# Kernel optimization log

Measured on AMD Instinct MI355X. Metric: run time of the kernel, lower is better.

Reference implementation:

```python
import jax, jax.numpy as jnp
jax.config.update('jax_enable_x64', True)
import numpy as np

B = 16          # samples per batch
PTS = 50000     # points per sample
PP = 2048       # pairs per sample
C = 64          # backbone_out_channels
HID = 1024      # mlp_hidden
MASK = 65535
RANK_MSE_WEIGHT = 0.1


def _hash4(idx):
    # pack (b, x, y, z) into one int64 key, 16 bits per field
    idx = idx.astype(jnp.int64)
    return ((idx[:, 0] & MASK) << 48) | ((idx[:, 1] & MASK) << 32) | ((idx[:, 2] & MASK) << 16) | (idx[:, 3] & MASK)


def setup_inputs() -> dict:
    key = jax.random.key(0)
    ks = jax.random.split(key, 8)
    N = B * PTS
    P = B * PP
    grid_coord = jax.random.randint(ks[0], (N, 3), 0, 1024, dtype=jnp.int32)
    offset = (jnp.arange(1, B + 1) * PTS).astype(jnp.int64)          # cumulative point ends
    batch = jnp.searchsorted(offset, jnp.arange(N), side='right')
    point_indices = jnp.concatenate([batch[:, None].astype(jnp.int32), grid_coord], axis=1)
    perm = jax.random.permutation(ks[1], N)
    voxel_indices = point_indices[perm].astype(jnp.int64)            # backbone._last_indices
    voxel_features = jax.random.normal(ks[2], (N, C), dtype=jnp.float32)
    pairs = jax.random.randint(ks[3], (P, 2), 0, PTS, dtype=jnp.int64)   # sample-local indices
    pair_reward = jax.random.uniform(ks[4], (P,), dtype=jnp.float32)
    pair_offset = (jnp.arange(1, B + 1) * PP).astype(jnp.int64)      # cumulative pair ends
    din = 3 * C
    def lin(k, fi, fo):
        return jax.random.normal(k, (fi, fo), dtype=jnp.float32) / np.float32(np.sqrt(fi))
    W1 = lin(ks[5], din, HID); b1 = jnp.zeros((HID,), jnp.float32)
    W2 = lin(ks[6], HID, HID); b2 = jnp.zeros((HID,), jnp.float32)
    W3 = lin(ks[7], HID, 1);   b3 = jnp.zeros((1,), jnp.float32)
    return dict(voxel_features=voxel_features, pair_reward=pair_reward,
                W1=W1, b1=b1, W2=W2, b2=b2, W3=W3, b3=b3,
                grid_coord=grid_coord, offset=offset, voxel_indices=voxel_indices,
                pairs=pairs, pair_offset=pair_offset)


def reference(voxel_features, pair_reward, W1, b1, W2, b2, W3, b3,
              grid_coord, offset, voxel_indices, pairs, pair_offset):
    N = grid_coord.shape[0]
    # --- match sparse voxel features back to point order (sort + searchsorted + gather) ---
    batch = jnp.searchsorted(offset, jnp.arange(N), side='right')
    point_keys = _hash4(jnp.concatenate([batch[:, None].astype(jnp.int32), grid_coord], axis=1))
    voxel_keys = _hash4(voxel_indices)
    order = jnp.argsort(voxel_keys)
    vk_sorted = voxel_keys[order]
    loc = jnp.clip(jnp.searchsorted(vk_sorted, point_keys), 0, N - 1)
    point_feat = voxel_features[order[loc]]                          # [N, C]
    # --- shift sample-local pair indices by per-sample point start (vectorized offsets) ---
    P = pairs.shape[0]
    seg = jnp.searchsorted(pair_offset, jnp.arange(P), side='right') # segment id per pair
    point_starts = jnp.concatenate([jnp.zeros((1,), offset.dtype), offset[:-1]])
    shifted = pairs + point_starts[seg][:, None]
    f0 = point_feat[shifted[:, 0]]
    f1 = point_feat[shifted[:, 1]]
    pair_feat = jnp.concatenate([f0, f1, f0 - f1], axis=1)           # [P, 3C]
    # --- MLP head ---
    h = jax.nn.relu(pair_feat @ W1 + b1)
    h = jax.nn.relu(h @ W2 + b2)
    pred = (h @ W3 + b3)[:, 0]                                       # [P]
    # --- pair_rank loss, batched over equal-sized segments ---
    Bn = pair_offset.shape[0]
    Pp = P // Bn
    pb = pred.reshape(Bn, Pp)
    tb = pair_reward.reshape(Bn, Pp)
    dp = pb[:, :, None] - pb[:, None, :]                             # [B, Pp, Pp]
    dt = tb[:, :, None] - tb[:, None, :]
    sgn = jnp.sign(dt)
    triu = jnp.triu(jnp.ones((Pp, Pp), bool), 1)
    valid = triu[None, :, :] & (sgn != 0)
    sp = jax.nn.softplus(-sgn * dp)
    cnt = valid.sum(axis=(1, 2))
    rank_per = jnp.where(valid, sp, 0.0).sum(axis=(1, 2)) / jnp.maximum(cnt, 1)
    has = cnt > 0
    rank_loss = jnp.where(has, rank_per, 0.0).sum() / jnp.maximum(has.sum(), 1)
    mse_loss = jnp.mean((pb - tb) ** 2, axis=1).mean()
    loss = rank_loss + RANK_MSE_WEIGHT * mse_loss
    return loss
```

## Files before the change

### kernel.cpp

```cpp
#include <hip/hip_runtime.h>
#include <stdint.h>

#define BATCH   16
#define PTS     50000
#define PP      2048
#define NPTS    (BATCH*PTS)
#define NPAIR   (BATCH*PP)
#define NEND    (2*NPAIR)
#define CFEAT   64
#define KIN     128
#define HID     1024
#define QTS_LOG2 17
#define QTS     (1u<<QTS_LOG2)
#define QTS_MASK (QTS-1)
#define EMPTY_KEY 0xFFFFFFFFFFFFFFFFULL
#define NJB     64
#define RJ      (PP/NJB)

typedef unsigned long long ull;
typedef __attribute__((ext_vector_type(4))) float f32x4;
typedef __attribute__((ext_vector_type(8))) short bf16x8;

__device__ __forceinline__ ull mix64(ull h) {
  h ^= h >> 33; h *= 0xff51afd7ed558ccdULL;
  h ^= h >> 33; h *= 0xc4ceb9fe1a85ec53ULL;
  h ^= h >> 33; return h;
}

__device__ __forceinline__ unsigned short f2b(float x) {
  unsigned u = __float_as_uint(x);
  unsigned r = (u + 0x7FFFu + ((u >> 16) & 1u)) >> 16;
  return (unsigned short)r;
}

__global__ __launch_bounds__(256) void setup_kernel(
    ull* __restrict__ qtable, unsigned int* __restrict__ ans,
    const float* __restrict__ W1, unsigned short* __restrict__ Wt1,
    const float* __restrict__ W2, unsigned short* __restrict__ Wt2) {
  __shared__ unsigned short tile[32][33];
  int bid = blockIdx.x;
  int t = threadIdx.x;
  if (bid < 512) {
    int i = bid * 256 + t;
    qtable[i] = EMPTY_KEY;
    ans[i] = 0xFFFFFFFFu;
  } else if (bid < 1024) {
    int idx = (bid - 512) * 256 + t;
    int n = idx >> 7, k = idx & 127;
    float v;
    if (k < 64)
      v = W1[(size_t)k * HID + n] + W1[(size_t)(128 + k) * HID + n];
    else
      v = W1[(size_t)k * HID + n] - W1[(size_t)(64 + k) * HID + n];
    Wt1[(size_t)n * KIN + k] = f2b(v);
  } else {
    int b = bid - 1024;
    int nb = (b & 31) * 32, kb = (b >> 5) * 32;
    int tx = t & 31, ty = t >> 5;
#pragma unroll
    for (int r = 0; r < 32; r += 8)
      tile[ty + r][tx] = f2b(W2[(size_t)(kb + ty + r) * HID + nb + tx]);
    __syncthreads();
#pragma unroll
    for (int r = 0; r < 32; r += 8)
      Wt2[(size_t)(nb + ty + r) * HID + kb + tx] = tile[tx][ty + r];
  }
}

__global__ void qinsert(const int* __restrict__ pairs, const int* __restrict__ gc,
                        ull* __restrict__ qtable, unsigned int* __restrict__ eslot) {
  int e = blockIdx.x * blockDim.x + threadIdx.x;
  if (e >= NEND) return;
  int j = e >> 1, side = e & 1;
  int seg = j / PP;
  int pi = pairs[2*j + side] + seg * PTS;
  pi = pi < 0 ? 0 : (pi >= NPTS ? NPTS - 1 : pi);
  ull key = ((ull)seg << 30) | ((ull)(gc[3*pi] & 1023) << 20)
          | ((ull)(gc[3*pi+1] & 1023) << 10) | (ull)(gc[3*pi+2] & 1023);
  unsigned int h = (unsigned int)mix64(key) & QTS_MASK;
  for (int p = 0; p < (int)QTS; ++p) {
    ull prev = atomicCAS(&qtable[h], EMPTY_KEY, key);
    if (prev == EMPTY_KEY || prev == key) { eslot[e] = h; return; }
    h = (h + 1) & QTS_MASK;
  }
  eslot[e] = 0;
}

__global__ void vscan(const int* __restrict__ vidx, const ull* __restrict__ qtable,
                      unsigned int* __restrict__ ans) {
  int i = blockIdx.x * blockDim.x + threadIdx.x;
  if (i >= NPTS) return;
  int4 v = *(const int4*)&vidx[4*i];
  ull key = ((ull)(v.x & 31) << 30) | ((ull)(v.y & 1023) << 20)
          | ((ull)(v.z & 1023) << 10) | (ull)(v.w & 1023);
  unsigned int h = (unsigned int)mix64(key) & QTS_MASK;
  for (int p = 0; p < (int)QTS; ++p) {
    ull k = qtable[h];
    if (k == key) { atomicMin(&ans[h], (unsigned int)i); return; }
    if (k == EMPTY_KEY) return;
    h = (h + 1) & QTS_MASK;
  }
}

__global__ void gatherA(const float* __restrict__ vf,
                        const unsigned int* __restrict__ eslot,
                        const unsigned int* __restrict__ ans,
                        int jbase, unsigned short* __restrict__ Ab, int mrows) {
  int idx = blockIdx.x * 256 + threadIdx.x;
  if (idx >= mrows * 32) return;
  int j = idx >> 5, c4 = (idx & 31) * 4;
  int side = (c4 < 64) ? 0 : 1;
  unsigned int r = ans[eslot[2 * (jbase + j) + side]];
  r = r < (unsigned)NPTS ? r : 0u;
  int c = (c4 < 64) ? c4 : (c4 - 64);
  float4 v = *(const float4*)&vf[(size_t)r * CFEAT + c];
  ushort4 o;
  o.x = f2b(v.x); o.y = f2b(v.y); o.z = f2b(v.z); o.w = f2b(v.w);
  *(ushort4*)&Ab[(size_t)j * KIN + c4] = o;
}

template<bool FUSE>
__global__ __launch_bounds__(256) void gemm_mfma(
    const unsigned short* __restrict__ Ab, const unsigned short* __restrict__ Bt,
    const float* __restrict__ bias, const float* __restrict__ W3,
    unsigned short* __restrict__ Cb, float* __restrict__ partial,
    int M, int N, int K) {
  __shared__ unsigned short As[128 * 64];
  __shared__ unsigned short Bs[128 * 64];
  int t = threadIdx.x;
  int lane = t & 63, w = t >> 6;
  int l15 = lane & 15, lhi = lane >> 4;
  int wm = w >> 1, wn = w & 1;
  int ncol = gridDim.x;
  int stripe, cb;
  if ((gridDim.y & 7) == 0) {
    int h = blockIdx.x + ncol * blockIdx.y;
    stripe = (h & 7) + 8 * (h / (8 * ncol));
    cb = (h >> 3) % ncol;
  } else {
    stripe = blockIdx.y; cb = blockIdx.x;
  }
  int row0 = stripe * 128, col0 = cb * 128;
  size_t Kb = (size_t)K * 2;
  f32x4 acc[4][4] = {};
  const char* Ac = (const char*)As;
  const char* Bc = (const char*)Bs;
  for (int k0 = 0; k0 < K; k0 += 64) {
#pragma unroll
    for (int it = 0; it < 4; ++it) {
      int q = (it * 4 + w) * 64 + lane;
      int row = q >> 3, slot = q & 7;
      int sb = (slot * 16) ^ ((row & 7) << 4);
      const char* gA = (const char*)Ab + (size_t)(row0 + row) * Kb + (size_t)k0 * 2 + sb;
      const char* gB = (const char*)Bt + (size_t)(col0 + row) * Kb + (size_t)k0 * 2 + sb;
      char* lA = (char*)As + (it * 4 + w) * 1024;
      char* lB = (char*)Bs + (it * 4 + w) * 1024;
      __builtin_amdgcn_global_load_lds((const __attribute__((address_space(1))) void*)gA,
                                       (__attribute__((address_space(3))) void*)lA, 16, 0, 0);
      __builtin_amdgcn_global_load_lds((const __attribute__((address_space(1))) void*)gB,
                                       (__attribute__((address_space(3))) void*)lB, 16, 0, 0);
    }
    __syncthreads();
#pragma unroll
    for (int s = 0; s < 2; ++s) {
      bf16x8 af[4], bfr[4];
#pragma unroll
      for (int mi = 0; mi < 4; ++mi) {
        int row = wm * 64 + mi * 16 + l15;
        int off = row * 128 + ((s * 64 + lhi * 16) ^ ((row & 7) << 4));
        af[mi] = *(const bf16x8*)(Ac + off);
      }
#pragma unroll
      for (int ni = 0; ni < 4; ++ni) {
        int row = wn * 64 + ni * 16 + l15;
        int off = row * 128 + ((s * 64 + lhi * 16) ^ ((row & 7) << 4));
        bfr[ni] = *(const bf16x8*)(Bc + off);
      }
#pragma unroll
      for (int mi = 0; mi < 4; ++mi)
#pragma unroll
        for (int ni = 0; ni < 4; ++ni)
          acc[mi][ni] = __builtin_amdgcn_mfma_f32_16x16x32_bf16(af[mi], bfr[ni], acc[mi][ni], 0, 0, 0);
    }
    __syncthreads();
  }
  if (!FUSE) {
#pragma unroll
    for (int ni = 0; ni < 4; ++ni) {
      int col = col0 + wn * 64 + ni * 16 + l15;
      float bv = bias[col];
#pragma unroll
      for (int mi = 0; mi < 4; ++mi)
#pragma unroll
        for (int r = 0; r < 4; ++r) {
          int row = row0 + wm * 64 + mi * 16 + lhi * 4 + r;
          Cb[(size_t)row * N + col] = f2b(fmaxf(acc[mi][ni][r] + bv, 0.f));
        }
    }
  } else {
    float bb[4], ww[4];
#pragma unroll
    for (int ni = 0; ni < 4; ++ni) {
      int col = col0 + wn * 64 + ni * 16 + l15;
      bb[ni] = bias[col];
      ww[ni] = W3[col];
    }
#pragma unroll
    for (int mi = 0; mi < 4; ++mi)
#pragma unroll
      for (int r = 0; r < 4; ++r) {
        float pv = 0.f;
#pragma unroll
        for (int ni = 0; ni < 4; ++ni)
          pv += fmaxf(acc[mi][ni][r] + bb[ni], 0.f) * ww[ni];
        pv += __shfl_xor(pv, 1);
        pv += __shfl_xor(pv, 2);
        pv += __shfl_xor(pv, 4);
        pv += __shfl_xor(pv, 8);
        if (l15 == 0) {
          int row = row0 + wm * 64 + mi * 16 + lhi * 4 + r;
          partial[(size_t)row * 16 + cb * 2 + wn] = pv;
        }
      }
  }
}

#define BARF() do { asm volatile("" ::: "memory"); __builtin_amdgcn_s_barrier(); \
                    asm volatile("" ::: "memory"); } while (0)
#define Q_MFMA(MIB, NIB)                                                         \
  do {                                                                           \
    __builtin_amdgcn_s_setprio(1);                                               \
    _Pragma("unroll")                                                            \
    for (int mi = 0; mi < 4; ++mi)                                               \
      _Pragma("unroll")                                                          \
      for (int ni = 0; ni < 2; ++ni)                                             \
        _Pragma("unroll")                                                        \
        for (int s = 0; s < 2; ++s)                                              \
          acc[(MIB)*4 + mi][(NIB)*2 + ni] = __builtin_amdgcn_mfma_f32_16x16x32_bf16( \
              af[mi][s], bfr[(NIB)*2 + ni][s], acc[(MIB)*4 + mi][(NIB)*2 + ni], 0, 0, 0); \
    __builtin_amdgcn_s_setprio(0);                                               \
  } while (0)

__global__ __launch_bounds__(512, 2) void gemm2_8phase(
    const unsigned short* __restrict__ Ab, const unsigned short* __restrict__ Bt,
    const float* __restrict__ bias, const float* __restrict__ W3,
    float* __restrict__ partial, int M, int N, int K) {
  __shared__ char SM[131072];
  const int t = threadIdx.x;
  const int lane = t & 63;
  const int w = t >> 6;
  const int l15 = lane & 15, lhi = lane >> 4;
  const int wm = w >> 2, wn = w & 3;
  const int ncol = gridDim.x;
  const int h = blockIdx.x + ncol * blockIdx.y;
  const int stripe = (h & 7) + 8 * (h / (8 * ncol));
  const int cb = (h >> 3) % ncol;
  const int row0 = stripe * 256, col0 = cb * 256;
  const size_t Kb = (size_t)K * 2;
  const int nt = K >> 6;

  f32x4 acc[8][4] = {};

  auto STA = [&](int bq, int qa, int kt) {
    int rho = t >> 3, slot = t & 7;
    const char* g = (const char*)Ab + (size_t)(row0 + qa * 64 + rho) * Kb
                    + (size_t)kt * 128 + ((slot * 16) ^ ((rho & 7) << 4));
    char* l = SM + bq * 32768 + qa * 8192 + t * 16;
    __builtin_amdgcn_global_load_lds((const __attribute__((address_space(1))) void*)g,
                                     (__attribute__((address_space(3))) void*)l, 16, 0, 0);
  };
  auto STB = [&](int bq, int qb, int kt) {
    int rho = t >> 3, slot = t & 7;
    const char* g = (const char*)Bt + (size_t)(col0 + qb * 64 + rho) * Kb
                    + (size_t)kt * 128 + ((slot * 16) ^ ((rho & 7) << 4));
    char* l = SM + 65536 + bq * 32768 + qb * 8192 + t * 16;
    __builtin_amdgcn_global_load_lds((const __attribute__((address_space(1))) void*)g,
                                     (__attribute__((address_space(3))) void*)l, 16, 0, 0);
  };
  auto LDA = [&](int bq, int mi, int s) -> bf16x8 {
    int r = wm * 128 + mi * 16 + l15;
    int rho = r & 63;
    return *(const bf16x8*)(SM + bq * 32768 + (r >> 6) * 8192 + rho * 128
                            + ((s * 64 + lhi * 16) ^ ((rho & 7) << 4)));
  };
  auto LDB = [&](int bq, int ni, int s) -> bf16x8 {
    int r = wn * 64 + ni * 16 + l15;
    int rho = r & 63;
    return *(const bf16x8*)(SM + 65536 + bq * 32768 + (r >> 6) * 8192 + rho * 128
                            + ((s * 64 + lhi * 16) ^ ((rho & 7) << 4)));
  };

  STA(0, 0, 0); STA(0, 2, 0); STB(0, 0, 0); STB(0, 1, 0);
  STA(0, 1, 0); STA(0, 3, 0); STB(0, 2, 0); STB(0, 3, 0);
  if (nt > 1) { STA(1, 0, 1); STA(1, 2, 1); STB(1, 0, 1); STB(1, 1, 1);
                STA(1, 1, 1); STA(1, 3, 1); }
  asm volatile("s_waitcnt vmcnt(6)" ::: "memory");
  __builtin_amdgcn_s_barrier();
  asm volatile("" ::: "memory");

  bf16x8 af[4][2], bfr[4][2];
  for (int tt = 0; tt < nt; ++tt) {
    const int bq = tt & 1, nb = bq ^ 1;
#pragma unroll
    for (int mi = 0; mi < 4; ++mi)
#pragma unroll
      for (int s = 0; s < 2; ++s) af[mi][s] = LDA(bq, mi, s);
#pragma unroll
    for (int ni = 0; ni < 4; ++ni)
#pragma unroll
      for (int s = 0; s < 2; ++s) bfr[ni][s] = LDB(bq, ni, s);
    if (tt + 1 < nt) { STB(nb, 2, tt + 1); STB(nb, 3, tt + 1); }
    BARF();
    Q_MFMA(0, 0);
    BARF();
    if (tt + 2 < nt) { STA(bq, 0, tt + 2); STA(bq, 2, tt + 2); }
    BARF();
    Q_MFMA(0, 1);
    BARF();
#pragma unroll
    for (int mi = 0; mi < 4; ++mi)
#pragma unroll
      for (int s = 0; s < 2; ++s) af[mi][s] = LDA(bq, 4 + mi, s);
    if (tt + 2 < nt) { STB(bq, 0, tt + 2); STB(bq, 1, tt + 2); }
    BARF();
    Q_MFMA(1, 0);
    BARF();
    if (tt + 2 < nt) { STA(bq, 1, tt + 2); STA(bq, 3, tt + 2); }
    BARF();
    Q_MFMA(1, 1);
    asm volatile("s_waitcnt vmcnt(6)" ::: "memory");
    BARF();
  }

  float bb[4], ww[4];
#pragma unroll
  for (int ni = 0; ni < 4; ++ni) {
    int col = col0 + wn * 64 + ni * 16 + l15;
    bb[ni] = bias[col];
    ww[ni] = W3[col];
  }
#pragma unroll
  for (int mi = 0; mi < 8; ++mi)
#pragma unroll
    for (int r = 0; r < 4; ++r) {
      float pv = 0.f;
#pragma unroll
      for (int ni = 0; ni < 4; ++ni)
        pv += fmaxf(acc[mi][ni][r] + bb[ni], 0.f) * ww[ni];
      pv += __shfl_xor(pv, 1);
      pv += __shfl_xor(pv, 2);
      pv += __shfl_xor(pv, 4);
      pv += __shfl_xor(pv, 8);
      if (l15 == 0) {
        int row = row0 + wm * 128 + mi * 16 + lhi * 4 + r;
        partial[(size_t)row * 16 + cb * 4 + wn] = pv;
      }
    }
}

__global__ __launch_bounds__(256) void rank_kernel(
    const float* __restrict__ partial, const float* __restrict__ b3,
    const float* __restrict__ rew,
    double* __restrict__ rank_part, unsigned int* __restrict__ cnt_part,
    double* __restrict__ mse_part) {
  int b = blockIdx.x;
  int jb = blockIdx.y;
  __shared__ float pb[PP];
  __shared__ float tb[PP];
  int t = threadIdx.x;
  float b3v = b3[0];
  for (int i = t; i < PP; i += 256) {
    float s = b3v;
    const float* pr = &partial[(size_t)(b * PP + i) * 16];
#pragma unroll
    for (int nb = 0; nb < 16; ++nb) s += pr[nb];
    pb[i] = s;
    tb[i] = rew[b * PP + i];
  }
  __syncthreads();
  float tj[RJ], pj[RJ];
  int j0 = jb * RJ;
#pragma unroll
  for (int r = 0; r < RJ; ++r) { tj[r] = tb[j0 + r]; pj[r] = pb[j0 + r]; }
  float fs = 0.f;
  unsigned int c = 0;
  for (int i = j0 + 1 + t; i < PP; i += 256) {
    float ti = tb[i], pi = pb[i];
    int lim = i - j0;
#pragma unroll
    for (int r = 0; r < RJ; ++r) {
      float dt = ti - tj[r];
      float dp = pi - pj[r];
      float z = dt > 0.f ? -dp : dp;
      float e = __expf(-fabsf(z));
      float sp = fmaxf(z, 0.f) + __logf(1.f + e);
      bool v = (r < lim) && (dt != 0.f);
      fs += v ? sp : 0.f;
      c += v ? 1u : 0u;
    }
  }
  float msep = 0.f;
  if (jb == 0) {
    for (int i = t; i < PP; i += 256) {
      float d = pb[i] - tb[i];
      msep = fmaf(d, d, msep);
    }
  }
  __shared__ double sred[256];
  __shared__ unsigned int cred[256];
  __shared__ float mred[256];
  sred[t] = (double)fs; cred[t] = c; mred[t] = msep;
  __syncthreads();
  for (int off = 128; off > 0; off >>= 1) {
    if (t < off) {
      sred[t] += sred[t + off];
      cred[t] += cred[t + off];
      mred[t] += mred[t + off];
    }
    __syncthreads();
  }
  if (t == 0) {
    rank_part[b * NJB + jb] = sred[0];
    cnt_part[b * NJB + jb] = cred[0];
    if (jb == 0) mse_part[b] = (double)mred[0];
  }
}

__global__ void finalize_kernel(const double* __restrict__ rank_part,
                                const unsigned int* __restrict__ cnt_part,
                                const double* __restrict__ mse_part,
                                float* __restrict__ out) {
  __shared__ double rls[16];
  __shared__ double mss[16];
  __shared__ int hasv[16];
  int t = threadIdx.x;
  if (t < BATCH) {
    double s = 0.0;
    ull c = 0;
    for (int jb = 0; jb < NJB; ++jb) {
      s += rank_part[t * NJB + jb];
      c += cnt_part[t * NJB + jb];
    }
    rls[t] = c > 0 ? s / (double)c : 0.0;
    hasv[t] = c > 0 ? 1 : 0;
    mss[t] = mse_part[t] / (double)PP;
  }
  __syncthreads();
  if (t == 0) {
    double rl = 0.0, ms = 0.0;
    int has = 0;
    for (int b = 0; b < BATCH; ++b) { rl += rls[b]; has += hasv[b]; ms += mss[b]; }
    double rank_loss = rl / (double)(has > 0 ? has : 1);
    double mse_loss = ms / (double)BATCH;
    out[0] = (float)(rank_loss + 0.1 * mse_loss);
  }
}

extern "C" void kernel_launch(void* const* d_in, const int* in_sizes, int n_in,
                              void* d_out, int out_size, void* d_ws, size_t ws_size,
                              hipStream_t stream) {
  const float* vf   = (const float*)d_in[0];
  const float* rew  = (const float*)d_in[1];
  const float* W1   = (const float*)d_in[2];
  const float* b1   = (const float*)d_in[3];
  const float* W2   = (const float*)d_in[4];
  const float* b2   = (const float*)d_in[5];
  const float* W3   = (const float*)d_in[6];
  const float* b3   = (const float*)d_in[7];
  const int*   gc   = (const int*)d_in[8];
  const int*   vidx  = (const int*)d_in[10];
  const int*   pairs = (const int*)d_in[11];

  char* ws = (char*)d_ws;
  size_t off = 0;
  auto alloc = [&](size_t bytes) -> void* {
    void* p = ws + off;
    off += (bytes + 255) & ~(size_t)255;
    return p;
  };
  ull* qtable          = (ull*)alloc((size_t)QTS * 8);
  unsigned int* eslot  = (unsigned int*)alloc((size_t)NEND * 4);
  unsigned int* ans    = (unsigned int*)alloc((size_t)QTS * 4);
  float* partial       = (float*)alloc((size_t)NPAIR * 16 * 4);
  double* rank_part    = (double*)alloc((size_t)BATCH * NJB * 8);
  unsigned int* cnt_p  = (unsigned int*)alloc((size_t)BATCH * NJB * 4);
  double* mse_part     = (double*)alloc((size_t)BATCH * 8);
  unsigned short* Wt1  = (unsigned short*)alloc((size_t)HID * KIN * 2);
  unsigned short* Wt2  = (unsigned short*)alloc((size_t)HID * HID * 2);

  int mchunk = 2048;
  for (int cand = NPAIR; cand >= 2048; cand >>= 1) {
    size_t need = off + (size_t)cand * (KIN * 2 + HID * 2) + 2 * 65536;
    if (need <= ws_size) { mchunk = cand; break; }
  }
  unsigned short* Ab = (unsigned short*)alloc((size_t)mchunk * KIN * 2);
  unsigned short* h1 = (unsigned short*)alloc((size_t)mchunk * HID * 2);

  setup_kernel<<<2048, 256, 0, stream>>>(qtable, ans, W1, Wt1, W2, Wt2);
  qinsert<<<(NEND + 255) / 256, 256, 0, stream>>>(pairs, gc, qtable, eslot);
  vscan<<<(NPTS + 255) / 256, 256, 0, stream>>>(vidx, qtable, ans);

  int nchunk = NPAIR / mchunk;
  for (int ch = 0; ch < nchunk; ++ch) {
    gatherA<<<(mchunk * 32 + 255) / 256, 256, 0, stream>>>(
        vf, eslot, ans, ch * mchunk, Ab, mchunk);
    dim3 g1(HID / 128, mchunk / 128);
    gemm_mfma<false><<<g1, 256, 0, stream>>>(Ab, Wt1, b1, nullptr, h1, nullptr,
                                             mchunk, HID, KIN);
    if (mchunk >= 512 && (mchunk & 255) == 0) {
      dim3 g2(HID / 256, mchunk / 256);
      gemm2_8phase<<<g2, 512, 0, stream>>>(h1, Wt2, b2, W3,
                                           partial + (size_t)ch * mchunk * 16,
                                           mchunk, HID, HID);
    } else {
      dim3 g2(HID / 128, mchunk / 128);
      gemm_mfma<true><<<g2, 256, 0, stream>>>(h1, Wt2, b2, W3, nullptr,
                                              partial + (size_t)ch * mchunk * 16,
                                              mchunk, HID, HID);
    }
  }

  rank_kernel<<<dim3(BATCH, NJB), 256, 0, stream>>>(partial, b3, rew,
                                                    rank_part, cnt_p, mse_part);
  finalize_kernel<<<1, 64, 0, stream>>>(rank_part, cnt_p, mse_part, (float*)d_out);
}
```

Baseline: 181.9 us.

## Hash all voxels into a large table and probe it per pair-end in gatherA

The lookup is inverted. Instead of inserting the 65K pair endpoints into a small table and scanning all 800K voxels against it, every voxel is inserted into a 2M-slot table, and gatherA probes that table directly for each pair endpoint. This removes the qinsert kernel and the eslot indirection. The finalize kernel is also folded into rank_kernel through a last-block atomic counter. In exchange, setup must clear a much larger table (16MB keys plus 8MB values), and there are 800K atomic CAS inserts and redundant probes across the 32 threads of each pair row.

```diff
diff --git a/kernel.cpp b/kernel.cpp
--- a/kernel.cpp
+++ b/kernel.cpp
@@ -6,16 +6,16 @@
 #define PP      2048
 #define NPTS    (BATCH*PTS)
 #define NPAIR   (BATCH*PP)
-#define NEND    (2*NPAIR)
 #define CFEAT   64
 #define KIN     128
 #define HID     1024
-#define QTS_LOG2 17
-#define QTS     (1u<<QTS_LOG2)
-#define QTS_MASK (QTS-1)
+#define HTS_LOG2 21
+#define HTS     (1u<<HTS_LOG2)
+#define HTS_MASK (HTS-1)
 #define EMPTY_KEY 0xFFFFFFFFFFFFFFFFULL
 #define NJB     64
 #define RJ      (PP/NJB)
+#define NRANKBLK (BATCH*NJB)
 
 typedef unsigned long long ull;
 typedef __attribute__((ext_vector_type(4))) float f32x4;
@@ -34,18 +34,20 @@
 }
 
 __global__ __launch_bounds__(256) void setup_kernel(
-    ull* __restrict__ qtable, unsigned int* __restrict__ ans,
+    ull* __restrict__ hkeys, unsigned int* __restrict__ hvals,
     const float* __restrict__ W1, unsigned short* __restrict__ Wt1,
-    const float* __restrict__ W2, unsigned short* __restrict__ Wt2) {
+    const float* __restrict__ W2, unsigned short* __restrict__ Wt2,
+    unsigned int* __restrict__ counter) {
   __shared__ unsigned short tile[32][33];
   int bid = blockIdx.x;
   int t = threadIdx.x;
-  if (bid < 512) {
+  if (bid == 0 && t == 0) *counter = 0u;
+  if (bid < 8192) {
     int i = bid * 256 + t;
-    qtable[i] = EMPTY_KEY;
-    ans[i] = 0xFFFFFFFFu;
-  } else if (bid < 1024) {
-    int idx = (bid - 512) * 256 + t;
+    hkeys[i] = EMPTY_KEY;
+    hvals[i] = 0xFFFFFFFFu;
+  } else if (bid < 8704) {
+    int idx = (bid - 8192) * 256 + t;
     int n = idx >> 7, k = idx & 127;
     float v;
     if (k < 64)
@@ -54,7 +56,7 @@
       v = W1[(size_t)k * HID + n] - W1[(size_t)(64 + k) * HID + n];
     Wt1[(size_t)n * KIN + k] = f2b(v);
   } else {
-    int b = bid - 1024;
+    int b = bid - 8704;
     int nb = (b & 31) * 32, kb = (b >> 5) * 32;
     int tx = t & 31, ty = t >> 5;
 #pragma unroll
@@ -67,56 +69,53 @@
   }
 }
 
-__global__ void qinsert(const int* __restrict__ pairs, const int* __restrict__ gc,
-                        ull* __restrict__ qtable, unsigned int* __restrict__ eslot) {
-  int e = blockIdx.x * blockDim.x + threadIdx.x;
-  if (e >= NEND) return;
-  int j = e >> 1, side = e & 1;
-  int seg = j / PP;
-  int pi = pairs[2*j + side] + seg * PTS;
-  pi = pi < 0 ? 0 : (pi >= NPTS ? NPTS - 1 : pi);
-  ull key = ((ull)seg << 30) | ((ull)(gc[3*pi] & 1023) << 20)
-          | ((ull)(gc[3*pi+1] & 1023) << 10) | (ull)(gc[3*pi+2] & 1023);
-  unsigned int h = (unsigned int)mix64(key) & QTS_MASK;
-  for (int p = 0; p < (int)QTS; ++p) {
-    ull prev = atomicCAS(&qtable[h], EMPTY_KEY, key);
-    if (prev == EMPTY_KEY || prev == key) { eslot[e] = h; return; }
-    h = (h + 1) & QTS_MASK;
-  }
-  eslot[e] = 0;
-}
-
-__global__ void vscan(const int* __restrict__ vidx, const ull* __restrict__ qtable,
-                      unsigned int* __restrict__ ans) {
-  int i = blockIdx.x * blockDim.x + threadIdx.x;
+__global__ void vbuild(const int* __restrict__ vidx,
+                       ull* __restrict__ hkeys, unsigned int* __restrict__ hvals) {
+  int i = blockIdx.x * 256 + threadIdx.x;
   if (i >= NPTS) return;
   int4 v = *(const int4*)&vidx[4*i];
   ull key = ((ull)(v.x & 31) << 30) | ((ull)(v.y & 1023) << 20)
           | ((ull)(v.z & 1023) << 10) | (ull)(v.w & 1023);
-  unsigned int h = (unsigned int)mix64(key) & QTS_MASK;
-  for (int p = 0; p < (int)QTS; ++p) {
-    ull k = qtable[h];
-    if (k == key) { atomicMin(&ans[h], (unsigned int)i); return; }
-    if (k == EMPTY_KEY) return;
-    h = (h + 1) & QTS_MASK;
+  unsigned int h = (unsigned int)mix64(key) & HTS_MASK;
+  for (int p = 0; p < (int)HTS; ++p) {
+    ull prev = atomicCAS(&hkeys[h], EMPTY_KEY, key);
+    if (prev == EMPTY_KEY || prev == key) {
+      atomicMin(&hvals[h], (unsigned int)i);
+      return;
+    }
+    h = (h + 1) & HTS_MASK;
   }
 }
 
 __global__ void gatherA(const float* __restrict__ vf,
-                        const unsigned int* __restrict__ eslot,
-                        const unsigned int* __restrict__ ans,
+                        const int* __restrict__ pairs, const int* __restrict__ gc,
+                        const ull* __restrict__ hkeys,
+                        const unsigned int* __restrict__ hvals,
                         int jbase, unsigned short* __restrict__ Ab, int mrows) {
   int idx = blockIdx.x * 256 + threadIdx.x;
   if (idx >= mrows * 32) return;
-  int j = idx >> 5, c4 = (idx & 31) * 4;
-  int side = (c4 < 64) ? 0 : 1;
-  unsigned int r = ans[eslot[2 * (jbase + j) + side]];
+  int j = idx >> 5, c4i = idx & 31;
+  int jj = jbase + j;
+  int side = (c4i < 16) ? 0 : 1;
+  int seg = jj >> 11;
+  int pi = pairs[2*jj + side] + seg * PTS;
+  pi = pi < 0 ? 0 : (pi >= NPTS ? NPTS - 1 : pi);
+  ull key = ((ull)seg << 30) | ((ull)(gc[3*pi] & 1023) << 20)
+          | ((ull)(gc[3*pi+1] & 1023) << 10) | (ull)(gc[3*pi+2] & 1023);
+  unsigned int h = (unsigned int)mix64(key) & HTS_MASK;
+  unsigned int r = 0u;
+  for (int p = 0; p < (int)HTS; ++p) {
+    ull k = hkeys[h];
+    if (k == key) { r = hvals[h]; break; }
+    if (k == EMPTY_KEY) break;
+    h = (h + 1) & HTS_MASK;
+  }
   r = r < (unsigned)NPTS ? r : 0u;
-  int c = (c4 < 64) ? c4 : (c4 - 64);
+  int c = (c4i & 15) * 4;
   float4 v = *(const float4*)&vf[(size_t)r * CFEAT + c];
   ushort4 o;
   o.x = f2b(v.x); o.y = f2b(v.y); o.z = f2b(v.z); o.w = f2b(v.w);
-  *(ushort4*)&Ab[(size_t)j * KIN + c4] = o;
+  *(ushort4*)&Ab[(size_t)j * KIN + c4i * 4] = o;
 }
 
 template<bool FUSE>
@@ -362,11 +361,19 @@
     const float* __restrict__ partial, const float* __restrict__ b3,
     const float* __restrict__ rew,
     double* __restrict__ rank_part, unsigned int* __restrict__ cnt_part,
-    double* __restrict__ mse_part) {
+    double* __restrict__ mse_part, unsigned int* __restrict__ counter,
+    float* __restrict__ out) {
   int b = blockIdx.x;
   int jb = blockIdx.y;
   __shared__ float pb[PP];
   __shared__ float tb[PP];
+  __shared__ double sred[256];
+  __shared__ unsigned int cred[256];
+  __shared__ float mred[256];
+  __shared__ bool lastblk;
+  __shared__ double rls[16];
+  __shared__ double mss[16];
+  __shared__ int hasv[16];
   int t = threadIdx.x;
   float b3v = b3[0];
   for (int i = t; i < PP; i += 256) {
@@ -406,9 +413,6 @@
       msep = fmaf(d, d, msep);
     }
   }
-  __shared__ double sred[256];
-  __shared__ unsigned int cred[256];
-  __shared__ float mred[256];
   sred[t] = (double)fs; cred[t] = c; mred[t] = msep;
   __syncthreads();
   for (int off = 128; off > 0; off >>= 1) {
@@ -423,33 +427,29 @@
     rank_part[b * NJB + jb] = sred[0];
     cnt_part[b * NJB + jb] = cred[0];
     if (jb == 0) mse_part[b] = (double)mred[0];
-  }
-}
-
-__global__ void finalize_kernel(const double* __restrict__ rank_part,
-                                const unsigned int* __restrict__ cnt_part,
-                                const double* __restrict__ mse_part,
-                                float* __restrict__ out) {
-  __shared__ double rls[16];
-  __shared__ double mss[16];
-  __shared__ int hasv[16];
-  int t = threadIdx.x;
+    __threadfence();
+    unsigned int old = atomicAdd(counter, 1u);
+    lastblk = (old == NRANKBLK - 1);
+  }
+  __syncthreads();
+  if (!lastblk) return;
+  __threadfence();
   if (t < BATCH) {
     double s = 0.0;
-    ull c = 0;
-    for (int jb = 0; jb < NJB; ++jb) {
-      s += rank_part[t * NJB + jb];
-      c += cnt_part[t * NJB + jb];
-    }
-    rls[t] = c > 0 ? s / (double)c : 0.0;
-    hasv[t] = c > 0 ? 1 : 0;
+    ull cc = 0;
+    for (int jj = 0; jj < NJB; ++jj) {
+      s += rank_part[t * NJB + jj];
+      cc += cnt_part[t * NJB + jj];
+    }
+    rls[t] = cc > 0 ? s / (double)cc : 0.0;
+    hasv[t] = cc > 0 ? 1 : 0;
     mss[t] = mse_part[t] / (double)PP;
   }
   __syncthreads();
   if (t == 0) {
     double rl = 0.0, ms = 0.0;
     int has = 0;
-    for (int b = 0; b < BATCH; ++b) { rl += rls[b]; has += hasv[b]; ms += mss[b]; }
+    for (int bb2 = 0; bb2 < BATCH; ++bb2) { rl += rls[bb2]; has += hasv[bb2]; ms += mss[bb2]; }
     double rank_loss = rl / (double)(has > 0 ? has : 1);
     double mse_loss = ms / (double)BATCH;
     out[0] = (float)(rank_loss + 0.1 * mse_loss);
@@ -478,13 +478,13 @@
     off += (bytes + 255) & ~(size_t)255;
     return p;
   };
-  ull* qtable          = (ull*)alloc((size_t)QTS * 8);
-  unsigned int* eslot  = (unsigned int*)alloc((size_t)NEND * 4);
-  unsigned int* ans    = (unsigned int*)alloc((size_t)QTS * 4);
+  ull* hkeys           = (ull*)alloc((size_t)HTS * 8);
+  unsigned int* hvals  = (unsigned int*)alloc((size_t)HTS * 4);
   float* partial       = (float*)alloc((size_t)NPAIR * 16 * 4);
   double* rank_part    = (double*)alloc((size_t)BATCH * NJB * 8);
   unsigned int* cnt_p  = (unsigned int*)alloc((size_t)BATCH * NJB * 4);
   double* mse_part     = (double*)alloc((size_t)BATCH * 8);
+  unsigned int* counter= (unsigned int*)alloc(256);
   unsigned short* Wt1  = (unsigned short*)alloc((size_t)HID * KIN * 2);
   unsigned short* Wt2  = (unsigned short*)alloc((size_t)HID * HID * 2);
 
@@ -496,14 +496,13 @@
   unsigned short* Ab = (unsigned short*)alloc((size_t)mchunk * KIN * 2);
   unsigned short* h1 = (unsigned short*)alloc((size_t)mchunk * HID * 2);
 
-  setup_kernel<<<2048, 256, 0, stream>>>(qtable, ans, W1, Wt1, W2, Wt2);
-  qinsert<<<(NEND + 255) / 256, 256, 0, stream>>>(pairs, gc, qtable, eslot);
-  vscan<<<(NPTS + 255) / 256, 256, 0, stream>>>(vidx, qtable, ans);
+  setup_kernel<<<9728, 256, 0, stream>>>(hkeys, hvals, W1, Wt1, W2, Wt2, counter);
+  vbuild<<<(NPTS + 255) / 256, 256, 0, stream>>>(vidx, hkeys, hvals);
 
   int nchunk = NPAIR / mchunk;
   for (int ch = 0; ch < nchunk; ++ch) {
     gatherA<<<(mchunk * 32 + 255) / 256, 256, 0, stream>>>(
-        vf, eslot, ans, ch * mchunk, Ab, mchunk);
+        vf, pairs, gc, hkeys, hvals, ch * mchunk, Ab, mchunk);
     dim3 g1(HID / 128, mchunk / 128);
     gemm_mfma<false><<<g1, 256, 0, stream>>>(Ab, Wt1, b1, nullptr, h1, nullptr,
                                              mchunk, HID, KIN);
@@ -520,7 +519,6 @@
     }
   }
 
-  rank_kernel<<<dim3(BATCH, NJB), 256, 0, stream>>>(partial, b3, rew,
-                                                    rank_part, cnt_p, mse_part);
-  finalize_kernel<<<1, 64, 0, stream>>>(rank_part, cnt_p, mse_part, (float*)d_out);
-}
+  rank_kernel<<<dim3(BATCH, NJB), 256, 0, stream>>>(
+      partial, b3, rew, rank_part, cnt_p, mse_part, counter, (float*)d_out);
+}
```

After: 259.8 us. +42.9%, slower.
